# Kernel optimization log

Measured on AMD Instinct MI355X. Metric: run time of the kernel, lower is better.

The kernel has to match this reference:

```python
import jax, jax.numpy as jnp
import numpy as np

B, H, W = 64, 512, 512
NUM_RINGS = 256  # = min(image_shape) // 2, the RingManager default


def _ring_bins():
    # center = fft_size // 2 (rfft=False path)
    cy, cx = H // 2, W // 2
    Y, X = np.meshgrid(np.arange(H), np.arange(W), indexing='ij')
    R = np.sqrt((X - cx) ** 2 + (Y - cy) ** 2)
    # mask r is (R >= r) & (R < r+1)  <=>  floor(R) == r
    bins = np.floor(R).astype(np.int32)
    bins = np.where(bins < NUM_RINGS, bins, NUM_RINGS)  # overflow bucket (dropped)
    return jnp.asarray(bins.reshape(-1))

_BINS = _ring_bins()


def setup_inputs() -> dict:
    key = jax.random.key(0)
    k1, k2, k3, k4 = jax.random.split(key, 4)
    shp = (B, H, W)
    return {
        'f1r': jax.random.normal(k1, shp, jnp.float32),
        'f1i': jax.random.normal(k2, shp, jnp.float32),
        'f2r': jax.random.normal(k3, shp, jnp.float32),
        'f2i': jax.random.normal(k4, shp, jnp.float32),
    }


def reference(f1r, f1i, f2r, f2i):
    # complex FFT planes, flattened over pixels: [B, H*W]
    F1 = jax.lax.complex(f1r, f1i).reshape(B, H * W)
    F2 = jax.lax.complex(f2r, f2i).reshape(B, H * W)

    def seg(d):  # per-ring reduction in one O(H*W) pass
        return jax.ops.segment_sum(d, _BINS, num_segments=NUM_RINGS + 1)

    cross = jax.vmap(seg)(F1 * jnp.conj(F2))[:, :NUM_RINGS]   # [B, R] complex
    p1 = jax.vmap(seg)(jnp.abs(F1) ** 2)[:, :NUM_RINGS]        # [B, R]
    p2 = jax.vmap(seg)(jnp.abs(F2) ** 2)[:, :NUM_RINGS]        # [B, R]

    num = jnp.abs(cross)
    den = jnp.sqrt(p1 * p2)
    den_safe = jnp.where(den == 0, 1.0, den)
    # nan_to_num(0/0) -> 0; num==0 whenever den==0 (same ring support)
    return jnp.where(den == 0, 0.0, num / den_safe)
```

## Files before the change

### kernel.cpp

```cpp
#include <hip/hip_runtime.h>
#include <stdint.h>

#define BATCH 64
#define HH 512
#define NR 256
#define BANDH 8
#define NBANDS (256 / BANDH)

__device__ __forceinline__ uint32_t lds_off(const void* p) {
    return (uint32_t)(uintptr_t)p;
}

__device__ __forceinline__ void lds_add4(uint32_t addr, float v0, float v1,
                                         float v2, float v3) {
    asm volatile(
        "ds_add_f32 %0, %1\n\t"
        "ds_add_f32 %0, %2 offset:1028\n\t"
        "ds_add_f32 %0, %3 offset:2056\n\t"
        "ds_add_f32 %0, %4 offset:3084"
        :: "v"(addr), "v"(v0), "v"(v1), "v"(v2), "v"(v3));
}

__device__ __forceinline__ void gl_add(float* p, float v) {
    asm volatile("global_atomic_add_f32 %0, %1, off"
                 :: "v"(p), "v"(v) : "memory");
}

__global__ __launch_bounds__(256) void frc_fold(
    const float* __restrict__ f1r, const float* __restrict__ f1i,
    const float* __restrict__ f2r, const float* __restrict__ f2i,
    float* __restrict__ gacc )
{
    __shared__ float s_acc[4 * 257];
    for (int i = threadIdx.x; i < 4 * 257; i += 256) s_acc[i] = 0.f;
    __syncthreads();

    const int b    = blockIdx.y;
    const int band = blockIdx.x;
    const int w    = threadIdx.x >> 6;
    const int lane = threadIdx.x & 63;
    const int dx   = w * 64 + lane;
    const int dx2  = dx * dx;
    const int wmin2 = (w * 64) * (w * 64);
    const float mx = (dx == 0) ? 0.f : 1.f;

    const int dy0 = band * BANDH;
    const size_t ib = (size_t)b * HH * HH;
    const uint32_t sbase = lds_off(s_acc);

    float acr = 0.f, aci = 0.f, ap1 = 0.f, ap2 = 0.f;
    int cur = -1;

    for (int dy = dy0; dy < dy0 + BANDH; ++dy) {
        if (wmin2 + dy * dy >= 65536) break;

        const int r2 = dx2 + dy * dy;
        int bin = (int)sqrtf((float)r2);
        bin -= (bin * bin > r2);
        bin += ((bin + 1) * (bin + 1) <= r2);
        if (bin > 256) bin = 256;

        const float my = (dy == 0) ? 0.f : 1.f;

        const size_t rp = ib + (size_t)(256 + dy) * HH;
        const size_t rm = ib + (size_t)(256 - dy) * HH;
        const int xp = 256 + dx;
        const int xm = 256 - dx;

        const float A1 = f1r[rp + xp], B1 = f1i[rp + xp];
        const float A2 = f2r[rp + xp], B2 = f2i[rp + xp];
        const float C1 = f1r[rp + xm], D1 = f1i[rp + xm];
        const float C2 = f2r[rp + xm], D2 = f2i[rp + xm];
        const float E1 = f1r[rm + xp], G1 = f1i[rm + xp];
        const float E2 = f2r[rm + xp], G2 = f2i[rm + xp];
        const float P1 = f1r[rm + xm], Q1 = f1i[rm + xm];
        const float P2 = f2r[rm + xm], Q2 = f2i[rm + xm];

        float scr = A1 * A2 + B1 * B2;
        float sci = B1 * A2 - A1 * B2;
        float sp1 = A1 * A1 + B1 * B1;
        float sp2 = A2 * A2 + B2 * B2;

        scr += mx * (C1 * C2 + D1 * D2);
        sci += mx * (D1 * C2 - C1 * D2);
        sp1 += mx * (C1 * C1 + D1 * D1);
        sp2 += mx * (C2 * C2 + D2 * D2);

        scr += my * (E1 * E2 + G1 * G2);
        sci += my * (G1 * E2 - E1 * G2);
        sp1 += my * (E1 * E1 + G1 * G1);
        sp2 += my * (E2 * E2 + G2 * G2);

        const float mxy = mx * my;
        scr += mxy * (P1 * P2 + Q1 * Q2);
        sci += mxy * (Q1 * P2 - P1 * Q2);
        sp1 += mxy * (P1 * P1 + Q1 * Q1);
        sp2 += mxy * (P2 * P2 + Q2 * Q2);

        if (bin != cur) {
            if (cur >= 0)
                lds_add4(sbase + 4u * (uint32_t)cur, acr, aci, ap1, ap2);
            acr = 0.f; aci = 0.f; ap1 = 0.f; ap2 = 0.f;
            cur = bin;
        }
        acr += scr; aci += sci; ap1 += sp1; ap2 += sp2;
    }
    if (cur >= 0)
        lds_add4(sbase + 4u * (uint32_t)cur, acr, aci, ap1, ap2);

    asm volatile("s_waitcnt lgkmcnt(0)" ::: "memory");
    __syncthreads();

    {
        const int r = threadIdx.x;
        const float v0 = s_acc[0 * 257 + r];
        const float v1 = s_acc[1 * 257 + r];
        const float v2 = s_acc[2 * 257 + r];
        const float v3 = s_acc[3 * 257 + r];
        if (v0 != 0.f || v1 != 0.f || v2 != 0.f || v3 != 0.f) {
            float* g = gacc + (size_t)b * 4 * NR + r;
            gl_add(g + 0 * NR, v0);
            gl_add(g + 1 * NR, v1);
            gl_add(g + 2 * NR, v2);
            gl_add(g + 3 * NR, v3);
        }
    }
}

__global__ __launch_bounds__(NR) void frc_finalize(
    const float* __restrict__ gacc, float* __restrict__ out)
{
    const int b = blockIdx.x;
    const int r = threadIdx.x;
    const float* g = gacc + (size_t)b * 4 * NR + r;
    const float cr = g[0 * NR], ci = g[1 * NR], p1 = g[2 * NR], p2 = g[3 * NR];
    const float num = sqrtf(cr * cr + ci * ci);
    const float den = sqrtf(p1 * p2);
    out[(size_t)b * NR + r] = (den == 0.f) ? 0.f : num / den;
}

extern "C" void kernel_launch(void* const* d_in, const int* in_sizes, int n_in,
                              void* d_out, int out_size, void* d_ws, size_t ws_size,
                              hipStream_t stream) {
    const float* f1r = (const float*)d_in[0];
    const float* f1i = (const float*)d_in[1];
    const float* f2r = (const float*)d_in[2];
    const float* f2i = (const float*)d_in[3];
    float* out  = (float*)d_out;
    float* gacc = (float*)d_ws;

    (void)in_sizes; (void)n_in; (void)out_size; (void)ws_size;

    hipMemsetAsync(gacc, 0, (size_t)BATCH * 4 * NR * sizeof(float), stream);

    dim3 grid(NBANDS, BATCH);
    frc_fold<<<grid, 256, 0, stream>>>(f1r, f1i, f2r, f2i, gacc);
    frc_finalize<<<dim3(BATCH), dim3(NR), 0, stream>>>(gacc, out);
}
```

Baseline: 244.9 us.

## Replace quadrant-folded scalar loads with row-tiled float4 vectorized loads

Drops the four-way symmetric fold, in which each thread gathered mirrored pixels with scalar loads (the mirrored x accesses run in descending address order). Each wave now reads contiguous 4-pixel float4 chunks across RPW rows of one half-row, keeps per-column bin accumulators, and flushes to LDS on bin change. The grid doubles to cover the full image and waves whose tile lies entirely outside radius 256 skip their loads. The cost is more LDS atomic flushes per thread, since four columns each track their own bin, and a larger register footprint under the added launch bound.

```diff
diff --git a/kernel.cpp b/kernel.cpp
--- a/kernel.cpp
+++ b/kernel.cpp
@@ -1,11 +1,13 @@
 #include <hip/hip_runtime.h>
 #include <stdint.h>
+#include <limits.h>
 
 #define BATCH 64
 #define HH 512
 #define NR 256
-#define BANDH 8
-#define NBANDS (256 / BANDH)
+#define RPW 4
+#define BAND (RPW * 2)
+#define NBANDS (HH / BAND)
 
 __device__ __forceinline__ uint32_t lds_off(const void* p) {
     return (uint32_t)(uintptr_t)p;
@@ -26,7 +28,7 @@
                  :: "v"(p), "v"(v) : "memory");
 }
 
-__global__ __launch_bounds__(256) void frc_fold(
+__global__ __launch_bounds__(256, 4) void frc_rows(
     const float* __restrict__ f1r, const float* __restrict__ f1i,
     const float* __restrict__ f2r, const float* __restrict__ f2i,
     float* __restrict__ gacc )
@@ -39,74 +41,86 @@
     const int band = blockIdx.x;
     const int w    = threadIdx.x >> 6;
     const int lane = threadIdx.x & 63;
-    const int dx   = w * 64 + lane;
-    const int dx2  = dx * dx;
-    const int wmin2 = (w * 64) * (w * 64);
-    const float mx = (dx == 0) ? 0.f : 1.f;
+    const int half   = w & 1;
+    const int rowset = w >> 1;
 
-    const int dy0 = band * BANDH;
-    const size_t ib = (size_t)b * HH * HH;
+    const int c0 = half * 256 + 4 * lane;
+    const int y0 = band * BAND + rowset * RPW;
+
+    int d2i[4];
+    #pragma unroll
+    for (int j = 0; j < 4; ++j) { const int d = c0 + j - 256; d2i[j] = d * d; }
+    const int mind2 = min(min(d2i[0], d2i[1]), min(d2i[2], d2i[3]));
+
+    int mindy2 = INT_MAX;
+    #pragma unroll
+    for (int t = 0; t < RPW; ++t) {
+        const int dy = y0 + t - 256;
+        mindy2 = min(mindy2, dy * dy);
+    }
+
     const uint32_t sbase = lds_off(s_acc);
 
-    float acr = 0.f, aci = 0.f, ap1 = 0.f, ap2 = 0.f;
-    int cur = -1;
+    if (mind2 + mindy2 < 65536) {
+        const size_t base = (size_t)b * HH * HH + (size_t)c0;
 
-    for (int dy = dy0; dy < dy0 + BANDH; ++dy) {
-        if (wmin2 + dy * dy >= 65536) break;
+        float4 A1[RPW], B1[RPW], A2[RPW], B2[RPW];
+        #pragma unroll
+        for (int t = 0; t < RPW; ++t) {
+            const size_t off = base + (size_t)(y0 + t) * HH;
+            A1[t] = *(const float4*)(f1r + off);
+            B1[t] = *(const float4*)(f1i + off);
+            A2[t] = *(const float4*)(f2r + off);
+            B2[t] = *(const float4*)(f2i + off);
+        }
 
-        const int r2 = dx2 + dy * dy;
-        int bin = (int)sqrtf((float)r2);
-        bin -= (bin * bin > r2);
-        bin += ((bin + 1) * (bin + 1) <= r2);
-        if (bin > 256) bin = 256;
+        float acc0[4], acc1[4], acc2[4], acc3[4];
+        int cur[4];
+        #pragma unroll
+        for (int j = 0; j < 4; ++j) {
+            cur[j] = -1;
+            acc0[j] = 0.f; acc1[j] = 0.f; acc2[j] = 0.f; acc3[j] = 0.f;
+        }
 
-        const float my = (dy == 0) ? 0.f : 1.f;
+        #pragma unroll
+        for (int t = 0; t < RPW; ++t) {
+            const int dy  = y0 + t - 256;
+            const int dy2 = dy * dy;
+            const float a1[4] = {A1[t].x, A1[t].y, A1[t].z, A1[t].w};
+            const float b1[4] = {B1[t].x, B1[t].y, B1[t].z, B1[t].w};
+            const float a2[4] = {A2[t].x, A2[t].y, A2[t].z, A2[t].w};
+            const float b2[4] = {B2[t].x, B2[t].y, B2[t].z, B2[t].w};
 
-        const size_t rp = ib + (size_t)(256 + dy) * HH;
-        const size_t rm = ib + (size_t)(256 - dy) * HH;
-        const int xp = 256 + dx;
-        const int xm = 256 - dx;
+            #pragma unroll
+            for (int j = 0; j < 4; ++j) {
+                const int r2 = d2i[j] + dy2;
+                int bin = (int)sqrtf((float)r2);
+                bin -= (bin * bin > r2);
+                bin += ((bin + 1) * (bin + 1) <= r2);
+                if (bin > 256) bin = 256;
 
-        const float A1 = f1r[rp + xp], B1 = f1i[rp + xp];
-        const float A2 = f2r[rp + xp], B2 = f2i[rp + xp];
-        const float C1 = f1r[rp + xm], D1 = f1i[rp + xm];
-        const float C2 = f2r[rp + xm], D2 = f2i[rp + xm];
-        const float E1 = f1r[rm + xp], G1 = f1i[rm + xp];
-        const float E2 = f2r[rm + xp], G2 = f2i[rm + xp];
-        const float P1 = f1r[rm + xm], Q1 = f1i[rm + xm];
-        const float P2 = f2r[rm + xm], Q2 = f2i[rm + xm];
+                const float cr = a1[j] * a2[j] + b1[j] * b2[j];
+                const float ci = b1[j] * a2[j] - a1[j] * b2[j];
+                const float p1 = a1[j] * a1[j] + b1[j] * b1[j];
+                const float p2 = a2[j] * a2[j] + b2[j] * b2[j];
 
-        float scr = A1 * A2 + B1 * B2;
-        float sci = B1 * A2 - A1 * B2;
-        float sp1 = A1 * A1 + B1 * B1;
-        float sp2 = A2 * A2 + B2 * B2;
+                if (bin != cur[j]) {
+                    if (cur[j] >= 0)
+                        lds_add4(sbase + 4u * (uint32_t)cur[j],
+                                 acc0[j], acc1[j], acc2[j], acc3[j]);
+                    acc0[j] = 0.f; acc1[j] = 0.f; acc2[j] = 0.f; acc3[j] = 0.f;
+                    cur[j] = bin;
+                }
+                acc0[j] += cr; acc1[j] += ci; acc2[j] += p1; acc3[j] += p2;
+            }
+        }
 
-        scr += mx * (C1 * C2 + D1 * D2);
-        sci += mx * (D1 * C2 - C1 * D2);
-        sp1 += mx * (C1 * C1 + D1 * D1);
-        sp2 += mx * (C2 * C2 + D2 * D2);
-
-        scr += my * (E1 * E2 + G1 * G2);
-        sci += my * (G1 * E2 - E1 * G2);
-        sp1 += my * (E1 * E1 + G1 * G1);
-        sp2 += my * (E2 * E2 + G2 * G2);
-
-        const float mxy = mx * my;
-        scr += mxy * (P1 * P2 + Q1 * Q2);
-        sci += mxy * (Q1 * P2 - P1 * Q2);
-        sp1 += mxy * (P1 * P1 + Q1 * Q1);
-        sp2 += mxy * (P2 * P2 + Q2 * Q2);
-
-        if (bin != cur) {
-            if (cur >= 0)
-                lds_add4(sbase + 4u * (uint32_t)cur, acr, aci, ap1, ap2);
-            acr = 0.f; aci = 0.f; ap1 = 0.f; ap2 = 0.f;
-            cur = bin;
-        }
-        acr += scr; aci += sci; ap1 += sp1; ap2 += sp2;
+        #pragma unroll
+        for (int j = 0; j < 4; ++j)
+            if (cur[j] >= 0)
+                lds_add4(sbase + 4u * (uint32_t)cur[j],
+                         acc0[j], acc1[j], acc2[j], acc3[j]);
     }
-    if (cur >= 0)
-        lds_add4(sbase + 4u * (uint32_t)cur, acr, aci, ap1, ap2);
 
     asm volatile("s_waitcnt lgkmcnt(0)" ::: "memory");
     __syncthreads();
@@ -154,6 +168,6 @@
     hipMemsetAsync(gacc, 0, (size_t)BATCH * 4 * NR * sizeof(float), stream);
 
     dim3 grid(NBANDS, BATCH);
-    frc_fold<<<grid, 256, 0, stream>>>(f1r, f1i, f2r, f2i, gacc);
+    frc_rows<<<grid, 256, 0, stream>>>(f1r, f1i, f2r, f2i, gacc);
     frc_finalize<<<dim3(BATCH), dim3(NR), 0, stream>>>(gacc, out);
 }
```

New measurement: 404.0 us. +65.0%, slower.
